# Kernel tuning notes

Hardware: AMD Instinct MI355X
Metric: run time of the kernel (lower is better)

Reference implementation:

```python
import jax, jax.numpy as jnp
import numpy as np

DECAY = 0.8

def l2norm(t):
    # F.normalize with eps=1e-12
    n = jnp.linalg.norm(t, axis=-1, keepdims=True)
    return t / jnp.maximum(n, 1e-12)

def setup_inputs() -> dict:
    key = jax.random.key(0)
    k1, k2, k3 = jax.random.split(key, 3)
    x = jax.random.normal(k1, (16, 4096, 64), dtype=jnp.float32)
    embed = l2norm(jax.random.uniform(k2, (1, 4096, 64), dtype=jnp.float32) * 2.0 - 1.0)  # uniform_init + l2norm
    cluster_size = jax.random.uniform(k3, (1, 4096), dtype=jnp.float32) * 10.0
    return {"x": x, "embed": embed, "cluster_size": cluster_size}

def reference(x, embed, cluster_size):
    # x: [b, n, d] (ndim<4 -> add codebook dim), embed: [h, c, d]
    h, c, d = embed.shape
    xh = x[None, ...]                           # [1, b, n, d]
    shape = xh.shape
    flatten = l2norm(xh.reshape(h, -1, d))      # [h, N, d]
    embed_n = l2norm(embed)                     # [h, c, d]
    dist = jnp.einsum('hnd,hcd->hnc', flatten, embed_n)          # [h, N, c]
    embed_ind_flat = jnp.argmax(dist, axis=-1)                   # temperature==0 gumbel -> argmax
    embed_onehot = jax.nn.one_hot(embed_ind_flat, c, dtype=x.dtype)  # [h, N, c]
    embed_ind = embed_ind_flat.reshape(shape[:-1])               # [h, b, n]
    # batched_embedding: gather from the raw (non-normalized) codebook
    quantize = jax.vmap(lambda e, i: e[i])(embed, embed_ind_flat).reshape(shape)  # [h, b, n, d]
    # training-mode EMA codebook update (buffer updates returned as outputs)
    bins = embed_onehot.sum(axis=1)                              # [h, c]
    new_cluster_size = cluster_size * DECAY + bins * (1.0 - DECAY)
    zero_mask = bins == 0
    bins_safe = jnp.where(zero_mask, 1.0, bins)
    embed_sum = jnp.einsum('hnd,hnc->hcd', flatten, embed_onehot)  # [h, c, d]
    embed_normalized = l2norm(embed_sum / bins_safe[..., None])
    embed_normalized = jnp.where(zero_mask[..., None], embed_n, embed_normalized)
    new_embed = embed * DECAY + embed_normalized * (1.0 - DECAY)
    # squeeze back the added codebook dim (needs_codebook_dim path)
    return quantize[0], embed_ind[0], new_embed, new_cluster_size
```

## Files before the change

kernel.cpp:

```cpp
#include <hip/hip_runtime.h>
#include <math.h>

#define DECAY 0.8f
constexpr int B_     = 16;
constexpr int NSEQ   = 4096;
constexpr int D      = 64;
constexpr int C      = 4096;
constexpr int N      = B_ * NSEQ;
constexpr int NCHUNK = 4;
constexpr int CCHUNK = C / NCHUNK;
constexpr int PANEL  = 64;
constexpr int NPANEL = CCHUNK / PANEL;
constexpr int TILE_ELEMS = 32 * D;

#define GATE_THR  3e-4f
#define CONS_THR  1e-3f

typedef __attribute__((ext_vector_type(8)))  short bf16x8;
typedef __attribute__((ext_vector_type(16))) float f32x16;

__device__ __forceinline__ unsigned short bf16_rn(float f) {
    unsigned u = __builtin_bit_cast(unsigned, f);
    u += 0x7FFFu + ((u >> 16) & 1u);
    return (unsigned short)(u >> 16);
}
__device__ __forceinline__ float bf16_to_f(unsigned short h) {
    unsigned u = ((unsigned)h) << 16;
    return __builtin_bit_cast(float, u);
}
__device__ __forceinline__ f32x16 mfma32(bf16x8 a, bf16x8 b, f32x16 c) {
    return __builtin_amdgcn_mfma_f32_32x32x16_bf16(a, b, c, 0, 0, 0);
}
__device__ __forceinline__ void gload_lds16(const unsigned short* g,
                                            unsigned short* l) {
    __builtin_amdgcn_global_load_lds(
        (const __attribute__((address_space(1))) unsigned int*)g,
        (__attribute__((address_space(3))) unsigned int*)l, 16, 0, 0);
}

__global__ __launch_bounds__(256) void prep_e_kernel(
    const float* __restrict__ embed,
    float* __restrict__ embed_n,
    unsigned short* __restrict__ e_hi,
    unsigned short* __restrict__ e_lo,
    float* __restrict__ embed_sum,
    float* __restrict__ bins,
    int* __restrict__ dirty_count)
{
    int code = blockIdx.x * 4 + (threadIdx.x >> 6);
    int lane = threadIdx.x & 63;
    float v = embed[code * D + lane];
    float ss = v * v;
    #pragma unroll
    for (int o = 32; o > 0; o >>= 1) ss += __shfl_xor(ss, o);
    float inv = 1.0f / fmaxf(sqrtf(ss), 1e-12f);
    float en = v * inv;
    embed_n[code * D + lane] = en;

    unsigned short hi = bf16_rn(en);
    unsigned short lo = bf16_rn(en - bf16_to_f(hi));
    int t = code >> 5, r = code & 31;
    int g = lane >> 3, e = lane & 7;
    size_t pos = (size_t)t * TILE_ELEMS + (g * 32 + r) * 8 + e;
    e_hi[pos] = hi;
    e_lo[pos] = lo;

    embed_sum[code * D + lane] = 0.0f;
    if (lane == 0) bins[code] = 0.0f;
    if (blockIdx.x == 0 && threadIdx.x == 0) *dirty_count = 0;
}

__global__ __launch_bounds__(256) void assign_mfma_kernel(
    const float* __restrict__ x,
    const unsigned short* __restrict__ e_hi,
    const unsigned short* __restrict__ e_lo,
    float* __restrict__ part)
{
    __shared__ unsigned short lds_hi[2 * TILE_ELEMS];
    __shared__ unsigned short lds_lo[2 * TILE_ELEMS];

    const int tid  = threadIdx.x;
    const int lane = tid & 63;
    const int wid  = tid >> 6;
    const int m    = lane & 31;
    const int hi   = lane >> 5;
    const int rb   = (blockIdx.x * 4 + wid) * 32;
    const int cy   = blockIdx.y;

    bf16x8 xhi[4], xlo[4];
    #pragma unroll
    for (int c = 0; c < 4; ++c) {
        const float* p = x + (size_t)(rb + m) * D + c * 16 + hi * 8;
        float4 t0 = *(const float4*)p;
        float4 t1 = *(const float4*)(p + 4);
        float e[8] = {t0.x, t0.y, t0.z, t0.w, t1.x, t1.y, t1.z, t1.w};
        bf16x8 h, l2;
        #pragma unroll
        for (int j = 0; j < 8; ++j) {
            unsigned short hh = bf16_rn(e[j]);
            h[j]  = (short)hh;
            l2[j] = (short)bf16_rn(e[j] - bf16_to_f(hh));
        }
        xhi[c] = h;
        xlo[c] = l2;
    }

    float m1 = -3.4e38f, m2 = -3.4e38f;
    int   tl = 0;

    for (int p = 0; p < NPANEL; ++p) {
        const size_t pbase = ((size_t)cy * NPANEL + p) * (2 * TILE_ELEMS);
        __syncthreads();
        gload_lds16(e_hi + pbase + tid * 8,              &lds_hi[tid * 8]);
        gload_lds16(e_hi + pbase + TILE_ELEMS + tid * 8, &lds_hi[TILE_ELEMS + tid * 8]);
        gload_lds16(e_lo + pbase + tid * 8,              &lds_lo[tid * 8]);
        gload_lds16(e_lo + pbase + TILE_ELEMS + tid * 8, &lds_lo[TILE_ELEMS + tid * 8]);
        __syncthreads();

        #pragma unroll
        for (int t = 0; t < 2; ++t) {
            const int pt = (cy * NPANEL + p) * 2 + t;
            f32x16 accA = {}, accB = {};
            #pragma unroll
            for (int c = 0; c < 2; ++c) {
                const int off = t * TILE_ELEMS + ((c * 2 + hi) * 32 + m) * 8;
                bf16x8 eh = *(const bf16x8*)(lds_hi + off);
                bf16x8 el = *(const bf16x8*)(lds_lo + off);
                accA = mfma32(eh, xhi[c], accA);
                accA = mfma32(el, xhi[c], accA);
                accA = mfma32(eh, xlo[c], accA);
            }
            #pragma unroll
            for (int c = 2; c < 4; ++c) {
                const int off = t * TILE_ELEMS + ((c * 2 + hi) * 32 + m) * 8;
                bf16x8 eh = *(const bf16x8*)(lds_hi + off);
                bf16x8 el = *(const bf16x8*)(lds_lo + off);
                accB = mfma32(eh, xhi[c], accB);
                accB = mfma32(el, xhi[c], accB);
                accB = mfma32(eh, xlo[c], accB);
            }
            #pragma unroll
            for (int h = 0; h < 2; ++h) {
                float s0 = accA[h*8+0] + accB[h*8+0];
                float s1 = accA[h*8+1] + accB[h*8+1];
                float s2 = accA[h*8+2] + accB[h*8+2];
                float s3 = accA[h*8+3] + accB[h*8+3];
                float s4 = accA[h*8+4] + accB[h*8+4];
                float s5 = accA[h*8+5] + accB[h*8+5];
                float s6 = accA[h*8+6] + accB[h*8+6];
                float s7 = accA[h*8+7] + accB[h*8+7];
                float tm = fmaxf(fmaxf(fmaxf(s0, s1), fmaxf(s2, s3)),
                                 fmaxf(fmaxf(s4, s5), fmaxf(s6, s7)));
                const int ht = pt * 2 + h;
                float mn = fminf(m1, tm);
                bool  gt = tm > m1;
                tl = gt ? ht : tl;
                m1 = fmaxf(m1, tm);
                m2 = fmaxf(m2, mn);
            }
        }
    }

    {
        float b1 = __shfl_xor(m1, 32);
        float b2 = __shfl_xor(m2, 32);
        int   bt = __shfl_xor(tl, 32);
        float nm2 = fmaxf(fmaxf(m2, b2), fminf(m1, b1));
        bool  take = (b1 > m1);
        m1 = take ? b1 : m1;
        tl = take ? bt : tl;
        m2 = nm2;
    }
    if (lane < 32) {
        int row = rb + lane;
        float4 pr;
        pr.x = m1; pr.y = (float)tl; pr.z = m2; pr.w = 0.0f;
        *reinterpret_cast<float4*>(part + (size_t)row * D + cy * 4) = pr;
    }
}

__global__ __launch_bounds__(256) void merge_scatter_kernel(
    const float* __restrict__ x,
    const float* __restrict__ embed,
    const float* __restrict__ embed_n,
    float* __restrict__ q_out,
    float* __restrict__ ind_out,
    float* __restrict__ embed_sum,
    float* __restrict__ bins,
    int* __restrict__ dirty_count,
    int* __restrict__ dirty_list)
{
    int wid  = threadIdx.x >> 6;
    int lane = threadIdx.x & 63;
    int row  = blockIdx.x * 4 + wid;

    float w1a, m2x; int wt;
    {
        const float4* pp = reinterpret_cast<const float4*>(q_out + (size_t)row * D);
        float4 P = pp[0];
        w1a = P.x; wt = (int)P.y; m2x = P.z;
        #pragma unroll
        for (int j = 1; j < NCHUNK; ++j) {
            float4 Q = pp[j];
            float nm2 = fmaxf(fmaxf(m2x, Q.z), fminf(w1a, Q.x));
            if (Q.x > w1a) { w1a = Q.x; wt = (int)Q.y; }
            m2x = nm2;
        }
    }

    int   csub = lane >> 2;
    int   code = wt * 16 + csub;
    float dot;
    {
        const float4* ep = (const float4*)(embed_n + (size_t)code * D + (lane & 3) * 16);
        const float4* xp = (const float4*)(x + (size_t)row * D + (lane & 3) * 16);
        float a0 = 0.f, a1 = 0.f, a2 = 0.f, a3 = 0.f;
        #pragma unroll
        for (int k = 0; k < 4; ++k) {
            float4 e = ep[k], xx = xp[k];
            a0 = fmaf(e.x, xx.x, a0);
            a1 = fmaf(e.y, xx.y, a1);
            a2 = fmaf(e.z, xx.z, a2);
            a3 = fmaf(e.w, xx.w, a3);
        }
        dot = (a0 + a1) + (a2 + a3);
        dot += __shfl_xor(dot, 1);
        dot += __shfl_xor(dot, 2);
    }
    float v = dot, s = -3.4e38f;
    int   vi = code;
    #pragma unroll
    for (int d = 4; d <= 32; d <<= 1) {
        float bv = __shfl_xor(v, d);
        float bs = __shfl_xor(s, d);
        int   bi = __shfl_xor(vi, d);
        float ns = fmaxf(fmaxf(s, bs), fminf(v, bv));
        bool  take = (bv > v) || (bv == v && bi < vi);
        v  = take ? bv : v;
        vi = take ? bi : vi;
        s  = ns;
    }

    bool dirty = (v - m2x <= GATE_THR) || (fabsf(v - w1a) > CONS_THR);
    if (dirty) {
        if (lane == 0) {
            int slot = atomicAdd(dirty_count, 1);
            dirty_list[slot] = row;
        }
        return;
    }

    float xk = x[(size_t)row * D + lane];
    float ss = xk * xk;
    #pragma unroll
    for (int o = 32; o > 0; o >>= 1) ss += __shfl_xor(ss, o);
    float inv = 1.0f / fmaxf(sqrtf(ss), 1e-12f);

    if (lane == 0) {
        ind_out[row] = (float)vi;
        atomicAdd(&bins[vi], 1.0f);
    }
    q_out[(size_t)row * D + lane] = embed[(size_t)vi * D + lane];
    atomicAdd(&embed_sum[(size_t)vi * D + lane], xk * inv);
}

__global__ __launch_bounds__(256) void fallback_kernel(
    const float* __restrict__ x,
    const float* __restrict__ embed,
    const float* __restrict__ embed_n,
    const int* __restrict__ dirty_count,
    const int* __restrict__ dirty_list,
    float* __restrict__ ind_out,
    float* __restrict__ q_out,
    float* __restrict__ embed_sum,
    float* __restrict__ bins)
{
    __shared__ float xs[D];
    __shared__ float bv[256];
    __shared__ int   bidx[256];
    int cnt = *dirty_count;
    for (int i = blockIdx.x; i < cnt; i += gridDim.x) {
        int row = dirty_list[i];
        __syncthreads();
        if (threadIdx.x < D) xs[threadIdx.x] = x[(size_t)row * D + threadIdx.x];
        __syncthreads();
        float best = -3.4e38f;
        int   bi   = 0;
        int   c0   = threadIdx.x * 16;
        for (int c = c0; c < c0 + 16; ++c) {
            const float4* ep = (const float4*)(embed_n + (size_t)c * D);
            const float4* xp = (const float4*)xs;
            float a0 = 0.f, a1 = 0.f, a2 = 0.f, a3 = 0.f;
            #pragma unroll
            for (int k = 0; k < D / 4; ++k) {
                float4 e = ep[k], xx = xp[k];
                a0 = fmaf(e.x, xx.x, a0);
                a1 = fmaf(e.y, xx.y, a1);
                a2 = fmaf(e.z, xx.z, a2);
                a3 = fmaf(e.w, xx.w, a3);
            }
            float dd = (a0 + a1) + (a2 + a3);
            if (dd > best) { best = dd; bi = c; }
        }
        bv[threadIdx.x]   = best;
        bidx[threadIdx.x] = bi;
        __syncthreads();
        #pragma unroll
        for (int s = 128; s > 0; s >>= 1) {
            if (threadIdx.x < s) {
                float v2 = bv[threadIdx.x + s];
                int   i2 = bidx[threadIdx.x + s];
                if (v2 > bv[threadIdx.x] ||
                    (v2 == bv[threadIdx.x] && i2 < bidx[threadIdx.x])) {
                    bv[threadIdx.x]   = v2;
                    bidx[threadIdx.x] = i2;
                }
            }
            __syncthreads();
        }
        int fi = bidx[0];
        if (threadIdx.x == 0) {
            ind_out[row] = (float)fi;
            atomicAdd(&bins[fi], 1.0f);
        }
        if (threadIdx.x < 64) {
            float xk = xs[threadIdx.x];
            float ss = xk * xk;
            #pragma unroll
            for (int o = 32; o > 0; o >>= 1) ss += __shfl_xor(ss, o);
            float inv = 1.0f / fmaxf(sqrtf(ss), 1e-12f);
            q_out[(size_t)row * D + threadIdx.x] =
                embed[(size_t)fi * D + threadIdx.x];
            atomicAdd(&embed_sum[(size_t)fi * D + threadIdx.x], xk * inv);
        }
        __syncthreads();
    }
}

__global__ __launch_bounds__(256) void finalize_kernel(
    const float* __restrict__ embed,
    const float* __restrict__ cluster_size,
    const float* __restrict__ embed_n,
    const float* __restrict__ embed_sum,
    const float* __restrict__ bins,
    float* __restrict__ new_embed_out,
    float* __restrict__ new_cs_out)
{
    int code = blockIdx.x * 4 + (threadIdx.x >> 6);
    int lane = threadIdx.x & 63;
    float bsum = bins[code];
    if (lane == 0)
        new_cs_out[code] = cluster_size[code] * DECAY + bsum * (1.0f - DECAY);

    float en;
    if (bsum == 0.0f) {
        en = embed_n[code * D + lane];
    } else {
        float v = embed_sum[code * D + lane] / bsum;
        float ss = v * v;
        #pragma unroll
        for (int o = 32; o > 0; o >>= 1) ss += __shfl_xor(ss, o);
        en = v / fmaxf(sqrtf(ss), 1e-12f);
    }
    new_embed_out[code * D + lane] =
        embed[code * D + lane] * DECAY + en * (1.0f - DECAY);
}

extern "C" void kernel_launch(void* const* d_in, const int* in_sizes, int n_in,
                              void* d_out, int out_size, void* d_ws, size_t ws_size,
                              hipStream_t stream)
{
    const float* x            = (const float*)d_in[0];
    const float* embed        = (const float*)d_in[1];
    const float* cluster_size = (const float*)d_in[2];

    float* out     = (float*)d_out;
    float* q_out   = out;
    float* ind_out = out + (size_t)N * D;
    float* ne_out  = ind_out + N;
    float* ncs_out = ne_out + (size_t)C * D;

    char* ws = (char*)d_ws;
    float*          embed_n     = (float*)ws;
    float*          embed_sum   = (float*)(ws + (1u << 20));
    float*          bins        = (float*)(ws + (2u << 20));
    int*            dirty_list  = (int*)(ws + (2u << 20) + 65536);
    int*            dirty_count = (int*)(ws + (2u << 20) + 65536 + 262144);
    unsigned short* e_hi        = (unsigned short*)(ws + 3 * (1u << 20));
    unsigned short* e_lo        = (unsigned short*)(ws + 3 * (1u << 20) + 524288);

    prep_e_kernel<<<C / 4, 256, 0, stream>>>(embed, embed_n, e_hi, e_lo,
                                             embed_sum, bins, dirty_count);
    assign_mfma_kernel<<<dim3(N / 128, NCHUNK), 256, 0, stream>>>(
        x, e_hi, e_lo, q_out);
    merge_scatter_kernel<<<N / 4, 256, 0, stream>>>(x, embed, embed_n,
                                                    q_out, ind_out,
                                                    embed_sum, bins,
                                                    dirty_count, dirty_list);
    fallback_kernel<<<1024, 256, 0, stream>>>(x, embed, embed_n, dirty_count,
                                              dirty_list, ind_out, q_out,
                                              embed_sum, bins);
    finalize_kernel<<<C / 4, 256, 0, stream>>>(embed, cluster_size, embed_n,
                                               embed_sum, bins, ne_out, ncs_out);
}
```

Measured before the change: 183.3 us.

## Replicate scatter accumulators to cut atomic contention and enlarge assign blocks

The embed_sum and bins accumulators are replicated up to four times, selected by block index, so concurrent atomics spread across copies. The finalize kernel then sums the copies. Separately, the assign kernel moves to 512-thread blocks with 8 waves sharing each codebook panel in LDS, so each thread issues half as many global-to-LDS loads and panel reuse doubles. The costs are more zeroing work, extra reads in finalize, and a workspace layout that needs a size check.

```diff
diff --git a/kernel.cpp b/kernel.cpp
--- a/kernel.cpp
+++ b/kernel.cpp
@@ -45,7 +45,8 @@
     unsigned short* __restrict__ e_lo,
     float* __restrict__ embed_sum,
     float* __restrict__ bins,
-    int* __restrict__ dirty_count)
+    int* __restrict__ dirty_count,
+    int ncpy)
 {
     int code = blockIdx.x * 4 + (threadIdx.x >> 6);
     int lane = threadIdx.x & 63;
@@ -65,12 +66,14 @@
     e_hi[pos] = hi;
     e_lo[pos] = lo;
 
-    embed_sum[code * D + lane] = 0.0f;
-    if (lane == 0) bins[code] = 0.0f;
+    for (int k = 0; k < ncpy; ++k) {
+        embed_sum[(size_t)k * C * D + code * D + lane] = 0.0f;
+        if (lane == 0) bins[k * C + code] = 0.0f;
+    }
     if (blockIdx.x == 0 && threadIdx.x == 0) *dirty_count = 0;
 }
 
-__global__ __launch_bounds__(256) void assign_mfma_kernel(
+__global__ __launch_bounds__(512) void assign_mfma_kernel(
     const float* __restrict__ x,
     const unsigned short* __restrict__ e_hi,
     const unsigned short* __restrict__ e_lo,
@@ -84,7 +87,7 @@
     const int wid  = tid >> 6;
     const int m    = lane & 31;
     const int hi   = lane >> 5;
-    const int rb   = (blockIdx.x * 4 + wid) * 32;
+    const int rb   = (blockIdx.x * 8 + wid) * 32;
     const int cy   = blockIdx.y;
 
     bf16x8 xhi[4], xlo[4];
@@ -111,10 +114,8 @@
     for (int p = 0; p < NPANEL; ++p) {
         const size_t pbase = ((size_t)cy * NPANEL + p) * (2 * TILE_ELEMS);
         __syncthreads();
-        gload_lds16(e_hi + pbase + tid * 8,              &lds_hi[tid * 8]);
-        gload_lds16(e_hi + pbase + TILE_ELEMS + tid * 8, &lds_hi[TILE_ELEMS + tid * 8]);
-        gload_lds16(e_lo + pbase + tid * 8,              &lds_lo[tid * 8]);
-        gload_lds16(e_lo + pbase + TILE_ELEMS + tid * 8, &lds_lo[TILE_ELEMS + tid * 8]);
+        gload_lds16(e_hi + pbase + tid * 8, &lds_hi[tid * 8]);
+        gload_lds16(e_lo + pbase + tid * 8, &lds_lo[tid * 8]);
         __syncthreads();
 
         #pragma unroll
@@ -188,11 +189,13 @@
     float* __restrict__ embed_sum,
     float* __restrict__ bins,
     int* __restrict__ dirty_count,
-    int* __restrict__ dirty_list)
+    int* __restrict__ dirty_list,
+    int ncpy)
 {
     int wid  = threadIdx.x >> 6;
     int lane = threadIdx.x & 63;
     int row  = blockIdx.x * 4 + wid;
+    int cpy  = blockIdx.x & (ncpy - 1);
 
     float w1a, m2x; int wt;
     {
@@ -258,10 +261,10 @@
 
     if (lane == 0) {
         ind_out[row] = (float)vi;
-        atomicAdd(&bins[vi], 1.0f);
+        atomicAdd(&bins[cpy * C + vi], 1.0f);
     }
     q_out[(size_t)row * D + lane] = embed[(size_t)vi * D + lane];
-    atomicAdd(&embed_sum[(size_t)vi * D + lane], xk * inv);
+    atomicAdd(&embed_sum[(size_t)cpy * C * D + (size_t)vi * D + lane], xk * inv);
 }
 
 __global__ __launch_bounds__(256) void fallback_kernel(
@@ -273,12 +276,14 @@
     float* __restrict__ ind_out,
     float* __restrict__ q_out,
     float* __restrict__ embed_sum,
-    float* __restrict__ bins)
+    float* __restrict__ bins,
+    int ncpy)
 {
     __shared__ float xs[D];
     __shared__ float bv[256];
     __shared__ int   bidx[256];
     int cnt = *dirty_count;
+    int cpy = blockIdx.x & (ncpy - 1);
     for (int i = blockIdx.x; i < cnt; i += gridDim.x) {
         int row = dirty_list[i];
         __syncthreads();
@@ -321,7 +326,7 @@
         int fi = bidx[0];
         if (threadIdx.x == 0) {
             ind_out[row] = (float)fi;
-            atomicAdd(&bins[fi], 1.0f);
+            atomicAdd(&bins[cpy * C + fi], 1.0f);
         }
         if (threadIdx.x < 64) {
             float xk = xs[threadIdx.x];
@@ -331,7 +336,8 @@
             float inv = 1.0f / fmaxf(sqrtf(ss), 1e-12f);
             q_out[(size_t)row * D + threadIdx.x] =
                 embed[(size_t)fi * D + threadIdx.x];
-            atomicAdd(&embed_sum[(size_t)fi * D + threadIdx.x], xk * inv);
+            atomicAdd(&embed_sum[(size_t)cpy * C * D + (size_t)fi * D + threadIdx.x],
+                      xk * inv);
         }
         __syncthreads();
     }
@@ -344,11 +350,13 @@
     const float* __restrict__ embed_sum,
     const float* __restrict__ bins,
     float* __restrict__ new_embed_out,
-    float* __restrict__ new_cs_out)
+    float* __restrict__ new_cs_out,
+    int ncpy)
 {
     int code = blockIdx.x * 4 + (threadIdx.x >> 6);
     int lane = threadIdx.x & 63;
-    float bsum = bins[code];
+    float bsum = 0.0f;
+    for (int k = 0; k < ncpy; ++k) bsum += bins[k * C + code];
     if (lane == 0)
         new_cs_out[code] = cluster_size[code] * DECAY + bsum * (1.0f - DECAY);
 
@@ -356,7 +364,10 @@
     if (bsum == 0.0f) {
         en = embed_n[code * D + lane];
     } else {
-        float v = embed_sum[code * D + lane] / bsum;
+        float vsum = 0.0f;
+        for (int k = 0; k < ncpy; ++k)
+            vsum += embed_sum[(size_t)k * C * D + code * D + lane];
+        float v = vsum / bsum;
         float ss = v * v;
         #pragma unroll
         for (int o = 32; o > 0; o >>= 1) ss += __shfl_xor(ss, o);
@@ -382,24 +393,28 @@
 
     char* ws = (char*)d_ws;
     float*          embed_n     = (float*)ws;
-    float*          embed_sum   = (float*)(ws + (1u << 20));
+    unsigned short* e_hi        = (unsigned short*)(ws + (1u << 20));
+    unsigned short* e_lo        = (unsigned short*)(ws + (1u << 20) + 524288);
     float*          bins        = (float*)(ws + (2u << 20));
-    int*            dirty_list  = (int*)(ws + (2u << 20) + 65536);
-    int*            dirty_count = (int*)(ws + (2u << 20) + 65536 + 262144);
-    unsigned short* e_hi        = (unsigned short*)(ws + 3 * (1u << 20));
-    unsigned short* e_lo        = (unsigned short*)(ws + 3 * (1u << 20) + 524288);
+    int*            dirty_list  = (int*)(ws + (2u << 20) + 262144);
+    int*            dirty_count = (int*)(ws + (2u << 20) + 524288);
+    float*          embed_sum   = (float*)(ws + (3u << 20));
+
+    const size_t need4 = (3u << 20) + 4u * ((size_t)C * D * 4);
+    const int ncpy = (ws_size >= need4) ? 4 : 1;
 
     prep_e_kernel<<<C / 4, 256, 0, stream>>>(embed, embed_n, e_hi, e_lo,
-                                             embed_sum, bins, dirty_count);
-    assign_mfma_kernel<<<dim3(N / 128, NCHUNK), 256, 0, stream>>>(
+                                             embed_sum, bins, dirty_count, ncpy);
+    assign_mfma_kernel<<<dim3(N / 256, NCHUNK), 512, 0, stream>>>(
         x, e_hi, e_lo, q_out);
     merge_scatter_kernel<<<N / 4, 256, 0, stream>>>(x, embed, embed_n,
                                                     q_out, ind_out,
                                                     embed_sum, bins,
-                                                    dirty_count, dirty_list);
+                                                    dirty_count, dirty_list, ncpy);
     fallback_kernel<<<1024, 256, 0, stream>>>(x, embed, embed_n, dirty_count,
                                               dirty_list, ind_out, q_out,
-                                              embed_sum, bins);
+                                              embed_sum, bins, ncpy);
     finalize_kernel<<<C / 4, 256, 0, stream>>>(embed, cluster_size, embed_n,
-                                               embed_sum, bins, ne_out, ncs_out);
-}
+                                               embed_sum, bins, ne_out, ncs_out,
+                                               ncpy);
+}
```

After: 177.1 us. 3.4% less time.

## Replace float atomic scatter with counting-sort gather for codebook sums; enlarge assign blocks

Applied to the files above, without the earlier changes.

The per-element float atomicAdd accumulation of normalized x into embed_sum is replaced by a counting sort. Rows take a slot via an integer atomic on per-code counts, a single-block scan builds offsets, rows are scattered into sorted order, and each code's wave then sums its rows directly. The change removes heavy atomic contention on embed_sum and makes the sum order deterministic. It costs two extra kernel launches, a serial single-block scan, and a gather in which codes with many rows loop longer. The assign kernel also moves to 512-thread blocks with 128-code panels, so each panel load is shared by more waves.

```diff
diff --git a/kernel.cpp b/kernel.cpp
--- a/kernel.cpp
+++ b/kernel.cpp
@@ -9,7 +9,7 @@
 constexpr int N      = B_ * NSEQ;
 constexpr int NCHUNK = 4;
 constexpr int CCHUNK = C / NCHUNK;
-constexpr int PANEL  = 64;
+constexpr int PANEL  = 128;
 constexpr int NPANEL = CCHUNK / PANEL;
 constexpr int TILE_ELEMS = 32 * D;
 
@@ -43,8 +43,7 @@
     float* __restrict__ embed_n,
     unsigned short* __restrict__ e_hi,
     unsigned short* __restrict__ e_lo,
-    float* __restrict__ embed_sum,
-    float* __restrict__ bins,
+    int* __restrict__ cnt,
     int* __restrict__ dirty_count)
 {
     int code = blockIdx.x * 4 + (threadIdx.x >> 6);
@@ -65,26 +64,25 @@
     e_hi[pos] = hi;
     e_lo[pos] = lo;
 
-    embed_sum[code * D + lane] = 0.0f;
-    if (lane == 0) bins[code] = 0.0f;
+    if (lane == 0) cnt[code] = 0;
     if (blockIdx.x == 0 && threadIdx.x == 0) *dirty_count = 0;
 }
 
-__global__ __launch_bounds__(256) void assign_mfma_kernel(
+__global__ __launch_bounds__(512) void assign_mfma_kernel(
     const float* __restrict__ x,
     const unsigned short* __restrict__ e_hi,
     const unsigned short* __restrict__ e_lo,
     float* __restrict__ part)
 {
-    __shared__ unsigned short lds_hi[2 * TILE_ELEMS];
-    __shared__ unsigned short lds_lo[2 * TILE_ELEMS];
+    __shared__ unsigned short lds_hi[4 * TILE_ELEMS];
+    __shared__ unsigned short lds_lo[4 * TILE_ELEMS];
 
     const int tid  = threadIdx.x;
     const int lane = tid & 63;
     const int wid  = tid >> 6;
     const int m    = lane & 31;
     const int hi   = lane >> 5;
-    const int rb   = (blockIdx.x * 4 + wid) * 32;
+    const int rb   = (blockIdx.x * 8 + wid) * 32;
     const int cy   = blockIdx.y;
 
     bf16x8 xhi[4], xlo[4];
@@ -109,17 +107,17 @@
     int   tl = 0;
 
     for (int p = 0; p < NPANEL; ++p) {
-        const size_t pbase = ((size_t)cy * NPANEL + p) * (2 * TILE_ELEMS);
-        __syncthreads();
-        gload_lds16(e_hi + pbase + tid * 8,              &lds_hi[tid * 8]);
-        gload_lds16(e_hi + pbase + TILE_ELEMS + tid * 8, &lds_hi[TILE_ELEMS + tid * 8]);
-        gload_lds16(e_lo + pbase + tid * 8,              &lds_lo[tid * 8]);
-        gload_lds16(e_lo + pbase + TILE_ELEMS + tid * 8, &lds_lo[TILE_ELEMS + tid * 8]);
-        __syncthreads();
-
-        #pragma unroll
-        for (int t = 0; t < 2; ++t) {
-            const int pt = (cy * NPANEL + p) * 2 + t;
+        const size_t pbase = ((size_t)cy * NPANEL + p) * (4 * TILE_ELEMS);
+        __syncthreads();
+        gload_lds16(e_hi + pbase + tid * 8,        &lds_hi[tid * 8]);
+        gload_lds16(e_hi + pbase + 4096 + tid * 8, &lds_hi[4096 + tid * 8]);
+        gload_lds16(e_lo + pbase + tid * 8,        &lds_lo[tid * 8]);
+        gload_lds16(e_lo + pbase + 4096 + tid * 8, &lds_lo[4096 + tid * 8]);
+        __syncthreads();
+
+        #pragma unroll
+        for (int t = 0; t < 4; ++t) {
+            const int pt = (cy * NPANEL + p) * 4 + t;
             f32x16 accA = {}, accB = {};
             #pragma unroll
             for (int c = 0; c < 2; ++c) {
@@ -179,14 +177,14 @@
     }
 }
 
-__global__ __launch_bounds__(256) void merge_scatter_kernel(
+__global__ __launch_bounds__(256) void merge_rescan_kernel(
     const float* __restrict__ x,
     const float* __restrict__ embed,
     const float* __restrict__ embed_n,
     float* __restrict__ q_out,
     float* __restrict__ ind_out,
-    float* __restrict__ embed_sum,
-    float* __restrict__ bins,
+    int* __restrict__ cnt,
+    int* __restrict__ slot_arr,
     int* __restrict__ dirty_count,
     int* __restrict__ dirty_list)
 {
@@ -250,18 +248,11 @@
         return;
     }
 
-    float xk = x[(size_t)row * D + lane];
-    float ss = xk * xk;
-    #pragma unroll
-    for (int o = 32; o > 0; o >>= 1) ss += __shfl_xor(ss, o);
-    float inv = 1.0f / fmaxf(sqrtf(ss), 1e-12f);
-
     if (lane == 0) {
         ind_out[row] = (float)vi;
-        atomicAdd(&bins[vi], 1.0f);
+        slot_arr[row] = atomicAdd(&cnt[vi], 1);
     }
     q_out[(size_t)row * D + lane] = embed[(size_t)vi * D + lane];
-    atomicAdd(&embed_sum[(size_t)vi * D + lane], xk * inv);
 }
 
 __global__ __launch_bounds__(256) void fallback_kernel(
@@ -272,14 +263,14 @@
     const int* __restrict__ dirty_list,
     float* __restrict__ ind_out,
     float* __restrict__ q_out,
-    float* __restrict__ embed_sum,
-    float* __restrict__ bins)
+    int* __restrict__ cnt,
+    int* __restrict__ slot_arr)
 {
     __shared__ float xs[D];
     __shared__ float bv[256];
     __shared__ int   bidx[256];
-    int cnt = *dirty_count;
-    for (int i = blockIdx.x; i < cnt; i += gridDim.x) {
+    int n_d = *dirty_count;
+    for (int i = blockIdx.x; i < n_d; i += gridDim.x) {
         int row = dirty_list[i];
         __syncthreads();
         if (threadIdx.x < D) xs[threadIdx.x] = x[(size_t)row * D + threadIdx.x];
@@ -321,42 +312,83 @@
         int fi = bidx[0];
         if (threadIdx.x == 0) {
             ind_out[row] = (float)fi;
-            atomicAdd(&bins[fi], 1.0f);
-        }
-        if (threadIdx.x < 64) {
-            float xk = xs[threadIdx.x];
-            float ss = xk * xk;
-            #pragma unroll
-            for (int o = 32; o > 0; o >>= 1) ss += __shfl_xor(ss, o);
-            float inv = 1.0f / fmaxf(sqrtf(ss), 1e-12f);
+            slot_arr[row] = atomicAdd(&cnt[fi], 1);
+        }
+        if (threadIdx.x < 64)
             q_out[(size_t)row * D + threadIdx.x] =
                 embed[(size_t)fi * D + threadIdx.x];
-            atomicAdd(&embed_sum[(size_t)fi * D + threadIdx.x], xk * inv);
-        }
-        __syncthreads();
-    }
-}
-
-__global__ __launch_bounds__(256) void finalize_kernel(
+        __syncthreads();
+    }
+}
+
+__global__ __launch_bounds__(256) void scan_kernel(
+    const int* __restrict__ cnt,
+    int* __restrict__ offset)
+{
+    __shared__ int pre[256];
+    int base = threadIdx.x * 16;
+    int local[16];
+    int s = 0;
+    #pragma unroll
+    for (int i = 0; i < 16; ++i) { local[i] = s; s += cnt[base + i]; }
+    pre[threadIdx.x] = s;
+    __syncthreads();
+    if (threadIdx.x == 0) {
+        int a = 0;
+        for (int j = 0; j < 256; ++j) { int t = pre[j]; pre[j] = a; a += t; }
+    }
+    __syncthreads();
+    int p = pre[threadIdx.x];
+    #pragma unroll
+    for (int i = 0; i < 16; ++i) offset[base + i] = p + local[i];
+}
+
+__global__ __launch_bounds__(256) void scatter_rows_kernel(
+    const float* __restrict__ ind_out,
+    const int* __restrict__ slot_arr,
+    const int* __restrict__ offset,
+    int* __restrict__ sorted)
+{
+    int row  = blockIdx.x * 256 + threadIdx.x;
+    int code = (int)ind_out[row];
+    sorted[offset[code] + slot_arr[row]] = row;
+}
+
+__global__ __launch_bounds__(256) void sumfin_kernel(
+    const float* __restrict__ x,
     const float* __restrict__ embed,
     const float* __restrict__ cluster_size,
     const float* __restrict__ embed_n,
-    const float* __restrict__ embed_sum,
-    const float* __restrict__ bins,
+    const int* __restrict__ cnt,
+    const int* __restrict__ offset,
+    const int* __restrict__ sorted,
     float* __restrict__ new_embed_out,
     float* __restrict__ new_cs_out)
 {
     int code = blockIdx.x * 4 + (threadIdx.x >> 6);
     int lane = threadIdx.x & 63;
-    float bsum = bins[code];
+    int k    = cnt[code];
+    int off  = offset[code];
+
+    float acc = 0.0f;
+    for (int i = 0; i < k; ++i) {
+        int row = sorted[off + i];
+        float xv = x[(size_t)row * D + lane];
+        float ss = xv * xv;
+        #pragma unroll
+        for (int o = 32; o > 0; o >>= 1) ss += __shfl_xor(ss, o);
+        acc += xv * (1.0f / fmaxf(sqrtf(ss), 1e-12f));
+    }
+
+    float bsum = (float)k;
     if (lane == 0)
         new_cs_out[code] = cluster_size[code] * DECAY + bsum * (1.0f - DECAY);
 
     float en;
-    if (bsum == 0.0f) {
+    if (k == 0) {
         en = embed_n[code * D + lane];
     } else {
-        float v = embed_sum[code * D + lane] / bsum;
+        float v = acc / bsum;
         float ss = v * v;
         #pragma unroll
         for (int o = 32; o > 0; o >>= 1) ss += __shfl_xor(ss, o);
@@ -382,24 +414,30 @@
 
     char* ws = (char*)d_ws;
     float*          embed_n     = (float*)ws;
-    float*          embed_sum   = (float*)(ws + (1u << 20));
-    float*          bins        = (float*)(ws + (2u << 20));
-    int*            dirty_list  = (int*)(ws + (2u << 20) + 65536);
-    int*            dirty_count = (int*)(ws + (2u << 20) + 65536 + 262144);
-    unsigned short* e_hi        = (unsigned short*)(ws + 3 * (1u << 20));
-    unsigned short* e_lo        = (unsigned short*)(ws + 3 * (1u << 20) + 524288);
+    unsigned short* e_hi        = (unsigned short*)(ws + (1u << 20));
+    unsigned short* e_lo        = (unsigned short*)(ws + (1u << 20) + 524288);
+    int*            cnt         = (int*)(ws + (2u << 20));
+    int*            offset      = (int*)(ws + (2u << 20) + 16384);
+    int*            slot_arr    = (int*)(ws + (2u << 20) + 32768);
+    int*            sorted      = (int*)(ws + (2u << 20) + 32768 + 262144);
+    int*            dirty_list  = (int*)(ws + (2u << 20) + 32768 + 524288);
+    int*            dirty_count = (int*)(ws + (2u << 20) + 32768 + 786432);
 
     prep_e_kernel<<<C / 4, 256, 0, stream>>>(embed, embed_n, e_hi, e_lo,
-                                             embed_sum, bins, dirty_count);
-    assign_mfma_kernel<<<dim3(N / 128, NCHUNK), 256, 0, stream>>>(
+                                             cnt, dirty_count);
+    assign_mfma_kernel<<<dim3(N / 256, NCHUNK), 512, 0, stream>>>(
         x, e_hi, e_lo, q_out);
-    merge_scatter_kernel<<<N / 4, 256, 0, stream>>>(x, embed, embed_n,
-                                                    q_out, ind_out,
-                                                    embed_sum, bins,
-                                                    dirty_count, dirty_list);
+    merge_rescan_kernel<<<N / 4, 256, 0, stream>>>(x, embed, embed_n,
+                                                   q_out, ind_out, cnt,
+                                                   slot_arr, dirty_count,
+                                                   dirty_list);
     fallback_kernel<<<1024, 256, 0, stream>>>(x, embed, embed_n, dirty_count,
                                               dirty_list, ind_out, q_out,
-                                              embed_sum, bins);
-    finalize_kernel<<<C / 4, 256, 0, stream>>>(embed, cluster_size, embed_n,
-                                               embed_sum, bins, ne_out, ncs_out);
-}
+                                              cnt, slot_arr);
+    scan_kernel<<<1, 256, 0, stream>>>(cnt, offset);
+    scatter_rows_kernel<<<N / 256, 256, 0, stream>>>(ind_out, slot_arr,
+                                                     offset, sorted);
+    sumfin_kernel<<<C / 4, 256, 0, stream>>>(x, embed, cluster_size, embed_n,
+                                             cnt, offset, sorted,
+                                             ne_out, ncs_out);
+}
```

Result: slower. 200.2 us (+9.2%).
